# Performance work log

Hardware: AMD Instinct MI355X
Metric: run time of the kernel (lower is better)

## Reference

```python
import jax, jax.numpy as jnp
import numpy as np
import math

DIM = 1024
NHEADS = 8
HEAD_DIM = 128
MAXSEQLEN = 2048
THETA = 10000.0


def _rope_tables():
    # speed = theta ** (-(arange(0, dim, 2) / dim)), t = arange(maxseqlen)
    half = HEAD_DIM // 2
    speed = THETA ** (-(np.arange(0, HEAD_DIM, 2)[:half].astype(np.float32) / HEAD_DIM))
    t = np.arange(MAXSEQLEN, dtype=np.float32)
    freqs = np.outer(t, speed)  # [maxseqlen, head_dim//2]
    return jnp.asarray(np.cos(freqs)), jnp.asarray(np.sin(freqs))


def setup_inputs() -> dict:
    key = jax.random.key(0)
    kx, kqkv, kout = jax.random.split(key, 3)
    B, T = 2, 2048
    hdim = NHEADS * HEAD_DIM
    std = 0.5 * DIM ** (-0.5)
    bound = (3.0 ** 0.5) * std
    x = jax.random.normal(kx, (B, T, DIM), dtype=jnp.float32)
    qkv_proj = jax.random.uniform(kqkv, (3, hdim, DIM), dtype=jnp.float32,
                                  minval=-bound, maxval=bound)
    # nn.Linear(hdim, dim, bias=False) default init: U(-1/sqrt(hdim), 1/sqrt(hdim))
    wb = 1.0 / math.sqrt(hdim)
    w_out = jax.random.uniform(kout, (DIM, hdim), dtype=jnp.float32,
                               minval=-wb, maxval=wb)
    cos, sin = _rope_tables()
    return {"x": x, "qkv_proj": qkv_proj, "w_out": w_out, "cos": cos, "sin": sin}


def _apply_rope(u, cos, sin):
    # u: [B, T, H, D]; rotate adjacent pairs (complex multiply)
    B, T, H, D = u.shape
    u = u.reshape(B, T, H, D // 2, 2)
    c = cos[:T][None, :, None, :]  # [1, T, 1, D//2]
    s = sin[:T][None, :, None, :]
    re = u[..., 0] * c - u[..., 1] * s
    im = u[..., 0] * s + u[..., 1] * c
    return jnp.stack([re, im], axis=-1).reshape(B, T, H, D)


def reference(x, qkv_proj, w_out, cos, sin):
    B, T, D = x.shape
    # fused QKV projection: [B, T, 3, hdim] -> [B, T, 3, H, head_dim]
    qkv = jnp.einsum('btd,ahd->btah', x, qkv_proj)
    qkv = qkv.reshape(B, T, 3, NHEADS, HEAD_DIM)
    q, k, v = qkv[:, :, 0], qkv[:, :, 1], qkv[:, :, 2]
    q = _apply_rope(q, cos, sin)
    k = _apply_rope(k, cos, sin)
    scale = HEAD_DIM ** (-0.5)
    logits = jnp.einsum('btnh,bsnh->bnts', q, k) * scale  # [B, H, T, T]
    causal = jnp.tril(jnp.ones((T, T), dtype=bool))
    masked = jnp.where(causal[None, None], logits, -jnp.inf)
    attn = jax.nn.softmax(masked, axis=-1)
    out = jnp.einsum('bnts,bsnh->btnh', attn, v).reshape(B, T, -1)
    out = out @ w_out.T  # [B, T, dim]
    return out, attn
```

## Files before the change

### kernel.cpp

```cpp
#include <hip/hip_runtime.h>

typedef __attribute__((ext_vector_type(8))) short bf16x8;
typedef __attribute__((ext_vector_type(4))) short bf16x4;
typedef __attribute__((ext_vector_type(4))) float f32x4;

#define MFMA(a, b, c) __builtin_amdgcn_mfma_f32_16x16x32_bf16((a), (b), (c), 0, 0, 0)

__device__ __forceinline__ unsigned short f2bf(float f) {
  unsigned int x = __float_as_uint(f);
  return (unsigned short)((x + 0x7fffu + ((x >> 16) & 1u)) >> 16);
}
__device__ __forceinline__ unsigned int cvtpk(float lo, float hi) {
  unsigned int r;
  asm("v_cvt_pk_bf16_f32 %0, %1, %2" : "=v"(r) : "v"(lo), "v"(hi));
  return r;
}

constexpr int SEQ = 2048;
constexpr int NH = 8;
constexpr int DH = 128;
constexpr int DIM = 1024;
constexpr float SCALE = 0.08838834764831845f;

__global__ __launch_bounds__(256) void k_qkv_rope(
    const float* __restrict__ x, const float* __restrict__ wqkv,
    const float* __restrict__ cosT, const float* __restrict__ sinT,
    unsigned short* __restrict__ q, unsigned short* __restrict__ k,
    unsigned short* __restrict__ vT)
{
  __shared__ __align__(16) unsigned short As[128][40];
  __shared__ __align__(16) unsigned short Bs[128][40];
  const int tid = threadIdx.x;
  const int wave = tid >> 6, lane = tid & 63;
  const int fr = lane & 15, fq = lane >> 4;
  const int fk = fq * 8;
  const int wr = (wave >> 1) * 64, wc = (wave & 1) * 64;
  const int m0 = blockIdx.x * 128, n0 = blockIdx.y * 128;

  f32x4 zero4 = {0.f, 0.f, 0.f, 0.f};
  f32x4 acc[4][4];
  for (int i = 0; i < 4; ++i)
    for (int j = 0; j < 4; ++j) acc[i][j] = zero4;

  for (int kt = 0; kt < 32; ++kt) {
    const int k0 = kt * 32;
    __syncthreads();
#pragma unroll
    for (int j = 0; j < 4; ++j) {
      int f = j * 256 + tid;
      int row = f >> 3, c4 = (f & 7) * 4;
      f32x4 va = *(const f32x4*)(x + (m0 + row) * 1024 + k0 + c4);
      f32x4 vb = *(const f32x4*)(wqkv + (n0 + row) * 1024 + k0 + c4);
      uint2 ua, ub;
      ua.x = cvtpk(va[0], va[1]); ua.y = cvtpk(va[2], va[3]);
      ub.x = cvtpk(vb[0], vb[1]); ub.y = cvtpk(vb[2], vb[3]);
      *(uint2*)&As[row][c4] = ua;
      *(uint2*)&Bs[row][c4] = ub;
    }
    __syncthreads();
    bf16x8 af[4], bfr[4];
#pragma unroll
    for (int mi = 0; mi < 4; ++mi) af[mi] = *(const bf16x8*)&As[wr + mi * 16 + fr][fk];
#pragma unroll
    for (int ni = 0; ni < 4; ++ni) bfr[ni] = *(const bf16x8*)&Bs[wc + ni * 16 + fr][fk];
#pragma unroll
    for (int mi = 0; mi < 4; ++mi)
#pragma unroll
      for (int ni = 0; ni < 4; ++ni)
        acc[mi][ni] = MFMA(af[mi], bfr[ni], acc[mi][ni]);
  }

#pragma unroll
  for (int mi = 0; mi < 4; ++mi)
#pragma unroll
    for (int ni = 0; ni < 4; ++ni)
#pragma unroll
      for (int r = 0; r < 4; ++r) {
        float val = acc[mi][ni][r];
        float other = __shfl_xor(val, 1, 64);
        int m = m0 + wr + mi * 16 + fq * 4 + r;
        int n = n0 + wc + ni * 16 + fr;
        int a = n >> 10, feat = n & 1023;
        int hh = feat >> 7, dh = feat & 127;
        int bi = m >> 11, t = m & 2047;
        if (a == 2) {
          vT[((bi * NH + hh) * DH + dh) * SEQ + t] = f2bf(val);
        } else {
          float c = cosT[t * 64 + (dh >> 1)];
          float s = sinT[t * 64 + (dh >> 1)];
          float o = ((dh & 1) == 0) ? (val * c - other * s) : (other * s + val * c);
          unsigned short* dst = (a == 0) ? q : k;
          dst[((bi * NH + hh) * SEQ + t) * DH + dh] = f2bf(o);
        }
      }
}

__global__ __launch_bounds__(256) void k_attn(
    const unsigned short* __restrict__ q, const unsigned short* __restrict__ k,
    const unsigned short* __restrict__ vT,
    float* __restrict__ attn, unsigned short* __restrict__ heads)
{
  __shared__ __align__(16) unsigned short Kt[128][136];
  __shared__ __align__(16) unsigned short Vt[128][132];
  __shared__ __align__(16) unsigned short Esc[4][16][40];

  const int tid = threadIdx.x;
  const int wave = tid >> 6, lane = tid & 63;
  const int fr = lane & 15, fq = lane >> 4;
  const int fk = fq * 8;
  const int rt = (blockIdx.z == 0) ? (int)blockIdx.x : (31 - (int)blockIdx.x);
  const int row0 = rt * 64;
  const int hh = blockIdx.y, bi = blockIdx.z;
  const int bh = bi * NH + hh;
  const int r0 = row0 + wave * 16;
  const int wmax = r0 + 15;

  const unsigned short* qb = q + bh * SEQ * DH;
  const unsigned short* kb = k + bh * SEQ * DH;
  const unsigned short* vb = vT + bh * DH * SEQ;

  bf16x8 aq[4];
#pragma unroll
  for (int ks = 0; ks < 4; ++ks)
    aq[ks] = *(const bf16x8*)(qb + (r0 + fr) * DH + ks * 32 + fk);

  const int nph = (rt + 2) >> 1;
  float rs[4] = {0.f, 0.f, 0.f, 0.f};

  for (int ph = 0; ph < nph; ++ph) {
    const int c0 = ph * 128;
    __syncthreads();
#pragma unroll
    for (int j = 0; j < 8; ++j) {
      int f = j * 256 + tid;
      int r = f >> 4, c = (f & 15) * 8;
      *(bf16x8*)&Kt[r][c] = *(const bf16x8*)(kb + (c0 + r) * DH + c);
    }
    __syncthreads();
#pragma unroll
    for (int half = 0; half < 8; ++half) {
      int ch = c0 + half * 16;
      if (ch <= wmax) {
        f32x4 s = {0.f, 0.f, 0.f, 0.f};
#pragma unroll
        for (int ks = 0; ks < 4; ++ks) {
          bf16x8 bk = *(const bf16x8*)&Kt[half * 16 + fr][ks * 32 + fk];
          s = MFMA(aq[ks], bk, s);
        }
        int col = ch + fr;
#pragma unroll
        for (int r = 0; r < 4; ++r) {
          int row = r0 + fq * 4 + r;
          if (col <= row) rs[r] += __expf(s[r] * SCALE);
        }
      }
    }
  }

#pragma unroll
  for (int r = 0; r < 4; ++r)
#pragma unroll
    for (int msk = 1; msk < 16; msk <<= 1)
      rs[r] += __shfl_xor(rs[r], msk, 64);

  float inv[4];
#pragma unroll
  for (int r = 0; r < 4; ++r) inv[r] = 1.0f / rs[r];

  f32x4 pv[8];
  {
    f32x4 zero4 = {0.f, 0.f, 0.f, 0.f};
#pragma unroll
    for (int i = 0; i < 8; ++i) pv[i] = zero4;
  }

  for (int ph = 0; ph < nph; ++ph) {
    const int c0 = ph * 128;
    __syncthreads();
#pragma unroll
    for (int j = 0; j < 8; ++j) {
      int f = j * 256 + tid;
      int r = f >> 4, c = (f & 15) * 8;
      *(bf16x8*)&Kt[r][c] = *(const bf16x8*)(kb + (c0 + r) * DH + c);
      *(bf16x8*)&Vt[r][c] = *(const bf16x8*)(vb + r * SEQ + c0 + c);
    }
    __syncthreads();
#pragma unroll
    for (int chunk = 0; chunk < 4; ++chunk) {
#pragma unroll
      for (int h2 = 0; h2 < 2; ++h2) {
        const int half = chunk * 2 + h2;
        const int ch = c0 + half * 16;
        const bool live = (ch <= wmax);
        f32x4 s = {0.f, 0.f, 0.f, 0.f};
        if (live) {
#pragma unroll
          for (int ks = 0; ks < 4; ++ks) {
            bf16x8 bk = *(const bf16x8*)&Kt[half * 16 + fr][ks * 32 + fk];
            s = MFMA(aq[ks], bk, s);
          }
        }
        const int col = ch + fr;
#pragma unroll
        for (int r = 0; r < 4; ++r) {
          int row = r0 + fq * 4 + r;
          float p = (live && col <= row) ? __expf(s[r] * SCALE) * inv[r] : 0.f;
          __builtin_nontemporal_store(p, &attn[((size_t)bh * SEQ + row) * SEQ + col]);
          Esc[wave][fq * 4 + r][h2 * 16 + fr] = f2bf(p);
        }
      }
      bf16x8 ae = *(const bf16x8*)&Esc[wave][fr][fk];
#pragma unroll
      for (int ni = 0; ni < 8; ++ni) {
        bf16x8 bv = *(const bf16x8*)&Vt[ni * 16 + fr][chunk * 32 + fk];
        pv[ni] = MFMA(ae, bv, pv[ni]);
      }
    }
  }

#pragma unroll
  for (int ni = 0; ni < 8; ++ni)
#pragma unroll
    for (int r = 0; r < 4; ++r) {
      int row = r0 + fq * 4 + r;
      int dh = ni * 16 + fr;
      heads[(bi * SEQ + row) * DIM + hh * DH + dh] = f2bf(pv[ni][r]);
    }

  {
    const int zstart = nph * 128;
    f32x4 z4 = {0.f, 0.f, 0.f, 0.f};
#pragma unroll
    for (int rr = 0; rr < 4; ++rr) {
      int row = r0 + rr * 4 + fq;
      float* dst = attn + ((size_t)bh * SEQ + row) * SEQ;
      for (int c = zstart + fr * 4; c < SEQ; c += 64)
        __builtin_nontemporal_store(z4, (f32x4*)(dst + c));
    }
  }
}

__global__ __launch_bounds__(256) void k_outproj(
    const unsigned short* __restrict__ heads, const float* __restrict__ wout,
    float* __restrict__ out)
{
  __shared__ __align__(16) unsigned short As[128][40];
  __shared__ __align__(16) unsigned short Bs[128][40];
  const int tid = threadIdx.x;
  const int wave = tid >> 6, lane = tid & 63;
  const int fr = lane & 15, fq = lane >> 4;
  const int fk = fq * 8;
  const int wr = (wave >> 1) * 64, wc = (wave & 1) * 64;
  const int m0 = blockIdx.x * 128, n0 = blockIdx.y * 128;

  f32x4 zero4 = {0.f, 0.f, 0.f, 0.f};
  f32x4 acc[4][4];
  for (int i = 0; i < 4; ++i)
    for (int j = 0; j < 4; ++j) acc[i][j] = zero4;

  for (int kt = 0; kt < 32; ++kt) {
    const int k0 = kt * 32;
    __syncthreads();
#pragma unroll
    for (int j = 0; j < 2; ++j) {
      int f = j * 256 + tid;
      int row = f >> 2, c = (f & 3) * 8;
      *(bf16x8*)&As[row][c] = *(const bf16x8*)(heads + (m0 + row) * 1024 + k0 + c);
    }
#pragma unroll
    for (int j = 0; j < 4; ++j) {
      int f = j * 256 + tid;
      int row = f >> 3, c4 = (f & 7) * 4;
      f32x4 vb = *(const f32x4*)(wout + (n0 + row) * 1024 + k0 + c4);
      uint2 ub;
      ub.x = cvtpk(vb[0], vb[1]); ub.y = cvtpk(vb[2], vb[3]);
      *(uint2*)&Bs[row][c4] = ub;
    }
    __syncthreads();
    bf16x8 af[4], bfr[4];
#pragma unroll
    for (int mi = 0; mi < 4; ++mi) af[mi] = *(const bf16x8*)&As[wr + mi * 16 + fr][fk];
#pragma unroll
    for (int ni = 0; ni < 4; ++ni) bfr[ni] = *(const bf16x8*)&Bs[wc + ni * 16 + fr][fk];
#pragma unroll
    for (int mi = 0; mi < 4; ++mi)
#pragma unroll
      for (int ni = 0; ni < 4; ++ni)
        acc[mi][ni] = MFMA(af[mi], bfr[ni], acc[mi][ni]);
  }

#pragma unroll
  for (int mi = 0; mi < 4; ++mi)
#pragma unroll
    for (int ni = 0; ni < 4; ++ni)
#pragma unroll
      for (int r = 0; r < 4; ++r) {
        int m = m0 + wr + mi * 16 + fq * 4 + r;
        int n = n0 + wc + ni * 16 + fr;
        out[m * 1024 + n] = acc[mi][ni][r];
      }
}

extern "C" void kernel_launch(void* const* d_in, const int* in_sizes, int n_in,
                              void* d_out, int out_size, void* d_ws, size_t ws_size,
                              hipStream_t stream)
{
  const float* x    = (const float*)d_in[0];
  const float* wqkv = (const float*)d_in[1];
  const float* wout = (const float*)d_in[2];
  const float* cosT = (const float*)d_in[3];
  const float* sinT = (const float*)d_in[4];

  float* out  = (float*)d_out;
  float* attn = out + 4194304;
  unsigned short* ws = (unsigned short*)d_ws;
  unsigned short* q     = ws;
  unsigned short* kk    = ws + 4194304;
  unsigned short* vT    = ws + 8388608;
  unsigned short* heads = ws + 12582912;

  k_qkv_rope<<<dim3(32, 24), 256, 0, stream>>>(x, wqkv, cosT, sinT, q, kk, vT);
  k_attn<<<dim3(32, 8, 2), 256, 0, stream>>>(q, kk, vT, attn, heads);
  k_outproj<<<dim3(32, 8), 256, 0, stream>>>(heads, wout, out);
}
```

Baseline: 213.2 us.

## Give each attention wave two 16-row tiles and vectorize attn stores

The attention kernel now runs 2 waves per block instead of 4. Each wave computes two 16-row query tiles and reuses every K and V fragment loaded from LDS for two MFMAs. Probabilities are written to the attn output as 16-byte vector stores read back from the bf16 staging buffer, replacing per-element scalar stores. This cuts LDS fragment traffic and makes the large attn write more coalesced. In exchange there are fewer waves per CU, higher register pressure, and attn values are now rounded to bf16 precision before being stored as fp32.

```diff
diff --git a/kernel.cpp b/kernel.cpp
--- a/kernel.cpp
+++ b/kernel.cpp
@@ -9,6 +9,9 @@
 __device__ __forceinline__ unsigned short f2bf(float f) {
   unsigned int x = __float_as_uint(f);
   return (unsigned short)((x + 0x7fffu + ((x >> 16) & 1u)) >> 16);
+}
+__device__ __forceinline__ float bf2f(unsigned short u) {
+  return __uint_as_float(((unsigned int)u) << 16);
 }
 __device__ __forceinline__ unsigned int cvtpk(float lo, float hi) {
   unsigned int r;
@@ -95,14 +98,14 @@
       }
 }
 
-__global__ __launch_bounds__(256) void k_attn(
+__global__ __launch_bounds__(128, 1) void k_attn(
     const unsigned short* __restrict__ q, const unsigned short* __restrict__ k,
     const unsigned short* __restrict__ vT,
     float* __restrict__ attn, unsigned short* __restrict__ heads)
 {
   __shared__ __align__(16) unsigned short Kt[128][136];
   __shared__ __align__(16) unsigned short Vt[128][132];
-  __shared__ __align__(16) unsigned short Esc[4][16][40];
+  __shared__ __align__(16) unsigned short Esc[2][32][40];
 
   const int tid = threadIdx.x;
   const int wave = tid >> 6, lane = tid & 63;
@@ -112,27 +115,30 @@
   const int row0 = rt * 64;
   const int hh = blockIdx.y, bi = blockIdx.z;
   const int bh = bi * NH + hh;
-  const int r0 = row0 + wave * 16;
-  const int wmax = r0 + 15;
+  const int r0 = row0 + wave * 32;
+  const int wmax = r0 + 31;
 
   const unsigned short* qb = q + bh * SEQ * DH;
   const unsigned short* kb = k + bh * SEQ * DH;
   const unsigned short* vb = vT + bh * DH * SEQ;
 
-  bf16x8 aq[4];
-#pragma unroll
-  for (int ks = 0; ks < 4; ++ks)
-    aq[ks] = *(const bf16x8*)(qb + (r0 + fr) * DH + ks * 32 + fk);
+  bf16x8 aq0[4], aq1[4];
+#pragma unroll
+  for (int ks = 0; ks < 4; ++ks) {
+    aq0[ks] = *(const bf16x8*)(qb + (r0 + fr) * DH + ks * 32 + fk);
+    aq1[ks] = *(const bf16x8*)(qb + (r0 + 16 + fr) * DH + ks * 32 + fk);
+  }
 
   const int nph = (rt + 2) >> 1;
-  float rs[4] = {0.f, 0.f, 0.f, 0.f};
+  float rs0[4] = {0.f, 0.f, 0.f, 0.f};
+  float rs1[4] = {0.f, 0.f, 0.f, 0.f};
 
   for (int ph = 0; ph < nph; ++ph) {
     const int c0 = ph * 128;
     __syncthreads();
 #pragma unroll
-    for (int j = 0; j < 8; ++j) {
-      int f = j * 256 + tid;
+    for (int j = 0; j < 16; ++j) {
+      int f = j * 128 + tid;
       int r = f >> 4, c = (f & 15) * 8;
       *(bf16x8*)&Kt[r][c] = *(const bf16x8*)(kb + (c0 + r) * DH + c);
     }
@@ -141,17 +147,20 @@
     for (int half = 0; half < 8; ++half) {
       int ch = c0 + half * 16;
       if (ch <= wmax) {
-        f32x4 s = {0.f, 0.f, 0.f, 0.f};
+        f32x4 s0 = {0.f, 0.f, 0.f, 0.f};
+        f32x4 s1 = {0.f, 0.f, 0.f, 0.f};
 #pragma unroll
         for (int ks = 0; ks < 4; ++ks) {
           bf16x8 bk = *(const bf16x8*)&Kt[half * 16 + fr][ks * 32 + fk];
-          s = MFMA(aq[ks], bk, s);
+          s0 = MFMA(aq0[ks], bk, s0);
+          s1 = MFMA(aq1[ks], bk, s1);
         }
         int col = ch + fr;
 #pragma unroll
         for (int r = 0; r < 4; ++r) {
           int row = r0 + fq * 4 + r;
-          if (col <= row) rs[r] += __expf(s[r] * SCALE);
+          if (col <= row) rs0[r] += __expf(s0[r] * SCALE);
+          if (col <= row + 16) rs1[r] += __expf(s1[r] * SCALE);
         }
       }
     }
@@ -160,26 +169,31 @@
 #pragma unroll
   for (int r = 0; r < 4; ++r)
 #pragma unroll
-    for (int msk = 1; msk < 16; msk <<= 1)
-      rs[r] += __shfl_xor(rs[r], msk, 64);
-
-  float inv[4];
-#pragma unroll
-  for (int r = 0; r < 4; ++r) inv[r] = 1.0f / rs[r];
-
-  f32x4 pv[8];
+    for (int msk = 1; msk < 16; msk <<= 1) {
+      rs0[r] += __shfl_xor(rs0[r], msk, 64);
+      rs1[r] += __shfl_xor(rs1[r], msk, 64);
+    }
+
+  float inv0[4], inv1[4];
+#pragma unroll
+  for (int r = 0; r < 4; ++r) {
+    inv0[r] = 1.0f / rs0[r];
+    inv1[r] = 1.0f / rs1[r];
+  }
+
+  f32x4 pv0[8], pv1[8];
   {
     f32x4 zero4 = {0.f, 0.f, 0.f, 0.f};
 #pragma unroll
-    for (int i = 0; i < 8; ++i) pv[i] = zero4;
+    for (int i = 0; i < 8; ++i) { pv0[i] = zero4; pv1[i] = zero4; }
   }
 
   for (int ph = 0; ph < nph; ++ph) {
     const int c0 = ph * 128;
     __syncthreads();
 #pragma unroll
-    for (int j = 0; j < 8; ++j) {
-      int f = j * 256 + tid;
+    for (int j = 0; j < 16; ++j) {
+      int f = j * 128 + tid;
       int r = f >> 4, c = (f & 15) * 8;
       *(bf16x8*)&Kt[r][c] = *(const bf16x8*)(kb + (c0 + r) * DH + c);
       *(bf16x8*)&Vt[r][c] = *(const bf16x8*)(vb + r * SEQ + c0 + c);
@@ -192,28 +206,49 @@
         const int half = chunk * 2 + h2;
         const int ch = c0 + half * 16;
         const bool live = (ch <= wmax);
-        f32x4 s = {0.f, 0.f, 0.f, 0.f};
+        f32x4 s0 = {0.f, 0.f, 0.f, 0.f};
+        f32x4 s1 = {0.f, 0.f, 0.f, 0.f};
         if (live) {
 #pragma unroll
           for (int ks = 0; ks < 4; ++ks) {
             bf16x8 bk = *(const bf16x8*)&Kt[half * 16 + fr][ks * 32 + fk];
-            s = MFMA(aq[ks], bk, s);
+            s0 = MFMA(aq0[ks], bk, s0);
+            s1 = MFMA(aq1[ks], bk, s1);
           }
         }
         const int col = ch + fr;
 #pragma unroll
         for (int r = 0; r < 4; ++r) {
           int row = r0 + fq * 4 + r;
-          float p = (live && col <= row) ? __expf(s[r] * SCALE) * inv[r] : 0.f;
-          __builtin_nontemporal_store(p, &attn[((size_t)bh * SEQ + row) * SEQ + col]);
-          Esc[wave][fq * 4 + r][h2 * 16 + fr] = f2bf(p);
-        }
-      }
-      bf16x8 ae = *(const bf16x8*)&Esc[wave][fr][fk];
+          float p0 = (live && col <= row) ? __expf(s0[r] * SCALE) * inv0[r] : 0.f;
+          float p1 = (live && col <= row + 16) ? __expf(s1[r] * SCALE) * inv1[r] : 0.f;
+          Esc[wave][fq * 4 + r][h2 * 16 + fr] = f2bf(p0);
+          Esc[wave][16 + fq * 4 + r][h2 * 16 + fr] = f2bf(p1);
+        }
+      }
+      bf16x8 ae0 = *(const bf16x8*)&Esc[wave][fr][fk];
+      bf16x8 ae1 = *(const bf16x8*)&Esc[wave][16 + fr][fk];
+      {
+        float* a0 = attn + ((size_t)bh * SEQ + r0 + fr) * SEQ + c0 + chunk * 32 + fk;
+        float* a1 = a0 + 16 * SEQ;
+        f32x4 w0 = {bf2f((unsigned short)ae0[0]), bf2f((unsigned short)ae0[1]),
+                    bf2f((unsigned short)ae0[2]), bf2f((unsigned short)ae0[3])};
+        f32x4 w1 = {bf2f((unsigned short)ae0[4]), bf2f((unsigned short)ae0[5]),
+                    bf2f((unsigned short)ae0[6]), bf2f((unsigned short)ae0[7])};
+        f32x4 w2 = {bf2f((unsigned short)ae1[0]), bf2f((unsigned short)ae1[1]),
+                    bf2f((unsigned short)ae1[2]), bf2f((unsigned short)ae1[3])};
+        f32x4 w3 = {bf2f((unsigned short)ae1[4]), bf2f((unsigned short)ae1[5]),
+                    bf2f((unsigned short)ae1[6]), bf2f((unsigned short)ae1[7])};
+        __builtin_nontemporal_store(w0, (f32x4*)a0);
+        __builtin_nontemporal_store(w1, (f32x4*)(a0 + 4));
+        __builtin_nontemporal_store(w2, (f32x4*)a1);
+        __builtin_nontemporal_store(w3, (f32x4*)(a1 + 4));
+      }
 #pragma unroll
       for (int ni = 0; ni < 8; ++ni) {
         bf16x8 bv = *(const bf16x8*)&Vt[ni * 16 + fr][chunk * 32 + fk];
-        pv[ni] = MFMA(ae, bv, pv[ni]);
+        pv0[ni] = MFMA(ae0, bv, pv0[ni]);
+        pv1[ni] = MFMA(ae1, bv, pv1[ni]);
       }
     }
   }
@@ -224,14 +259,15 @@
     for (int r = 0; r < 4; ++r) {
       int row = r0 + fq * 4 + r;
       int dh = ni * 16 + fr;
-      heads[(bi * SEQ + row) * DIM + hh * DH + dh] = f2bf(pv[ni][r]);
+      heads[(bi * SEQ + row) * DIM + hh * DH + dh] = f2bf(pv0[ni][r]);
+      heads[(bi * SEQ + row + 16) * DIM + hh * DH + dh] = f2bf(pv1[ni][r]);
     }
 
   {
     const int zstart = nph * 128;
     f32x4 z4 = {0.f, 0.f, 0.f, 0.f};
 #pragma unroll
-    for (int rr = 0; rr < 4; ++rr) {
+    for (int rr = 0; rr < 8; ++rr) {
       int row = r0 + rr * 4 + fq;
       float* dst = attn + ((size_t)bh * SEQ + row) * SEQ;
       for (int c = zstart + fr * 4; c < SEQ; c += 64)
@@ -320,6 +356,6 @@
   unsigned short* heads = ws + 12582912;
 
   k_qkv_rope<<<dim3(32, 24), 256, 0, stream>>>(x, wqkv, cosT, sinT, q, kk, vT);
-  k_attn<<<dim3(32, 8, 2), 256, 0, stream>>>(q, kk, vT, attn, heads);
+  k_attn<<<dim3(32, 8, 2), 128, 0, stream>>>(q, kk, vT, attn, heads);
   k_outproj<<<dim3(32, 8), 256, 0, stream>>>(heads, wout, out);
 }
```

Measured after the change: 329.2 us. 1.54x slower.

## Transpose QK MFMA to keep probabilities in registers and vectorize attn stores

Applied to the files above, without the earlier changes.

Swaps the MFMA operand order so each lane holds one query row and four consecutive key columns. Probabilities can then be packed straight into the A operand of the PV MFMA, removing the per-wave LDS scratch round-trip. The V tile is stored in LDS with a permuted column order to match that packed layout. Attention stores become 16-byte vector nontemporal stores, and the row-sum reduction shrinks to two shuffles. The cost is extra index arithmetic and split 8-byte LDS writes for V.

```diff
diff --git a/kernel.cpp b/kernel.cpp
--- a/kernel.cpp
+++ b/kernel.cpp
@@ -102,7 +102,6 @@
 {
   __shared__ __align__(16) unsigned short Kt[128][136];
   __shared__ __align__(16) unsigned short Vt[128][132];
-  __shared__ __align__(16) unsigned short Esc[4][16][40];
 
   const int tid = threadIdx.x;
   const int wave = tid >> 6, lane = tid & 63;
@@ -114,6 +113,7 @@
   const int bh = bi * NH + hh;
   const int r0 = row0 + wave * 16;
   const int wmax = r0 + 15;
+  const int myrow = r0 + fr;
 
   const unsigned short* qb = q + bh * SEQ * DH;
   const unsigned short* kb = k + bh * SEQ * DH;
@@ -122,10 +122,10 @@
   bf16x8 aq[4];
 #pragma unroll
   for (int ks = 0; ks < 4; ++ks)
-    aq[ks] = *(const bf16x8*)(qb + (r0 + fr) * DH + ks * 32 + fk);
+    aq[ks] = *(const bf16x8*)(qb + myrow * DH + ks * 32 + fk);
 
   const int nph = (rt + 2) >> 1;
-  float rs[4] = {0.f, 0.f, 0.f, 0.f};
+  float rs = 0.f;
 
   for (int ph = 0; ph < nph; ++ph) {
     const int c0 = ph * 128;
@@ -145,27 +145,20 @@
 #pragma unroll
         for (int ks = 0; ks < 4; ++ks) {
           bf16x8 bk = *(const bf16x8*)&Kt[half * 16 + fr][ks * 32 + fk];
-          s = MFMA(aq[ks], bk, s);
-        }
-        int col = ch + fr;
+          s = MFMA(bk, aq[ks], s);
+        }
 #pragma unroll
         for (int r = 0; r < 4; ++r) {
-          int row = r0 + fq * 4 + r;
-          if (col <= row) rs[r] += __expf(s[r] * SCALE);
-        }
-      }
-    }
-  }
-
-#pragma unroll
-  for (int r = 0; r < 4; ++r)
-#pragma unroll
-    for (int msk = 1; msk < 16; msk <<= 1)
-      rs[r] += __shfl_xor(rs[r], msk, 64);
-
-  float inv[4];
-#pragma unroll
-  for (int r = 0; r < 4; ++r) inv[r] = 1.0f / rs[r];
+          int col = ch + fq * 4 + r;
+          if (col <= myrow) rs += __expf(s[r] * SCALE);
+        }
+      }
+    }
+  }
+
+  rs += __shfl_xor(rs, 16, 64);
+  rs += __shfl_xor(rs, 32, 64);
+  const float inv = 1.0f / rs;
 
   f32x4 pv[8];
   {
@@ -182,11 +175,19 @@
       int f = j * 256 + tid;
       int r = f >> 4, c = (f & 15) * 8;
       *(bf16x8*)&Kt[r][c] = *(const bf16x8*)(kb + (c0 + r) * DH + c);
-      *(bf16x8*)&Vt[r][c] = *(const bf16x8*)(vb + r * SEQ + c0 + c);
+      bf16x8 w = *(const bf16x8*)(vb + r * SEQ + c0 + c);
+      int cb = c & ~31, within = c & 31;
+      int s8 = (within >> 3) & 1, b0 = within >> 4;
+      int col0 = cb + 16 * s8 + 4 * b0;
+      bf16x4 lo = {w[0], w[1], w[2], w[3]};
+      bf16x4 hi = {w[4], w[5], w[6], w[7]};
+      *(bf16x4*)&Vt[r][col0] = lo;
+      *(bf16x4*)&Vt[r][col0 + 8] = hi;
     }
     __syncthreads();
 #pragma unroll
     for (int chunk = 0; chunk < 4; ++chunk) {
+      union { unsigned int u[4]; bf16x8 v8; } pa;
 #pragma unroll
       for (int h2 = 0; h2 < 2; ++h2) {
         const int half = chunk * 2 + h2;
@@ -197,23 +198,25 @@
 #pragma unroll
           for (int ks = 0; ks < 4; ++ks) {
             bf16x8 bk = *(const bf16x8*)&Kt[half * 16 + fr][ks * 32 + fk];
-            s = MFMA(aq[ks], bk, s);
+            s = MFMA(bk, aq[ks], s);
           }
         }
-        const int col = ch + fr;
+        float p[4];
 #pragma unroll
         for (int r = 0; r < 4; ++r) {
-          int row = r0 + fq * 4 + r;
-          float p = (live && col <= row) ? __expf(s[r] * SCALE) * inv[r] : 0.f;
-          __builtin_nontemporal_store(p, &attn[((size_t)bh * SEQ + row) * SEQ + col]);
-          Esc[wave][fq * 4 + r][h2 * 16 + fr] = f2bf(p);
-        }
-      }
-      bf16x8 ae = *(const bf16x8*)&Esc[wave][fr][fk];
+          int col = ch + fq * 4 + r;
+          p[r] = (live && col <= myrow) ? __expf(s[r] * SCALE) * inv : 0.f;
+        }
+        f32x4 p4 = {p[0], p[1], p[2], p[3]};
+        __builtin_nontemporal_store(
+            p4, (f32x4*)(attn + ((size_t)bh * SEQ + myrow) * SEQ + ch + fq * 4));
+        pa.u[h2 * 2] = cvtpk(p[0], p[1]);
+        pa.u[h2 * 2 + 1] = cvtpk(p[2], p[3]);
+      }
 #pragma unroll
       for (int ni = 0; ni < 8; ++ni) {
-        bf16x8 bv = *(const bf16x8*)&Vt[ni * 16 + fr][chunk * 32 + fk];
-        pv[ni] = MFMA(ae, bv, pv[ni]);
+        bf16x8 bv = *(const bf16x8*)&Vt[ni * 16 + fr][chunk * 32 + fq * 8];
+        pv[ni] = MFMA(pa.v8, bv, pv[ni]);
       }
     }
   }
```

Result: no change. 210.5 us (-1.3%).
